# Performance work log

Hardware: AMD Instinct MI355X
Metric: run time of the kernel (lower is better)

The kernel has to match this reference:

```python
import jax, jax.numpy as jnp
import numpy as np

B, N, D = 4, 1024, 1024
H, HD, G = 16, 64, 4          # num_heads, dim_heads, num_groups
KVH = H // G                   # kv heads = 4


def setup_inputs() -> dict:
    key = jax.random.key(0)
    ks = jax.random.split(key, 5)
    s = 0.02
    return {
        "x": jax.random.normal(ks[0], (B, N, D), jnp.float32),
        "Wq": jax.random.normal(ks[1], (D, H * HD), jnp.float32) * s,
        "Wkv": jax.random.normal(ks[2], (D, 2 * H * HD // G), jnp.float32) * s,
        "Wg": jax.random.normal(ks[3], (D, H * HD), jnp.float32) * s,
        "bg": jnp.zeros((H * HD,), jnp.float32),
        "Wo": jax.random.normal(ks[4], (H * HD, D), jnp.float32) * s,
    }


def reference(x, Wq, Wkv, Wg, bg, Wo):
    # QKV projections (no bias on q/kv/o; bias on gate)
    q = (x @ Wq).reshape(B, N, H, HD).transpose(0, 2, 1, 3)        # (B,H,N,HD)
    kv = x @ Wkv                                                    # (B,N,2*KVH*HD)
    k, v = jnp.split(kv, 2, axis=-1)
    k = k.reshape(B, N, KVH, HD).transpose(0, 2, 1, 3)             # (B,KVH,N,HD)
    v = v.reshape(B, N, KVH, HD).transpose(0, 2, 1, 3)
    # GQA: repeat_interleave kv heads to match query heads
    k = jnp.repeat(k, G, axis=1)                                    # (B,H,N,HD)
    v = jnp.repeat(v, G, axis=1)
    # scaled dot product attention
    scores = jnp.einsum("bhqd,bhkd->bhqk", q, k) / jnp.sqrt(jnp.float32(HD))
    attn = jax.nn.softmax(scores, axis=-1)
    out = jnp.einsum("bhqk,bhkd->bhqd", attn, v)                    # (B,H,N,HD)
    out = out.transpose(0, 2, 1, 3).reshape(B, N, H * HD)
    # elementwise gate then output projection
    gate = x @ Wg + bg
    return (gate * out) @ Wo
```

## Files before the change

### kernel.cpp

```cpp
#include <hip/hip_runtime.h>
#include <hip/hip_bf16.h>
#include <stdint.h>

#define BB 4
#define NN 1024
#define DD 1024
#define HH 16
#define HDIM 64
#define KVHH 4
#define MM (BB * NN)

typedef __hip_bfloat16 bf16;
typedef __attribute__((ext_vector_type(8))) short bf16x8;
typedef __attribute__((ext_vector_type(4))) float f32x4;

__device__ __forceinline__ float b2f(unsigned short u) {
  return __uint_as_float(((unsigned)u) << 16);
}
__device__ __forceinline__ unsigned short f2b(float x) {
  bf16 h = __float2bfloat16(x);
  unsigned short u;
  __builtin_memcpy(&u, &h, 2);
  return u;
}
__device__ __forceinline__ f32x4 mfma16(bf16x8 a, bf16x8 b, f32x4 c) {
  return __builtin_amdgcn_mfma_f32_16x16x32_bf16(a, b, c, 0, 0, 0);
}
__device__ __forceinline__ void gl_lds16(const short* g, short* l) {
  __builtin_amdgcn_global_load_lds(
      (const __attribute__((address_space(1))) unsigned*)g,
      (__attribute__((address_space(3))) unsigned*)l, 16, 0, 0);
}

__global__ __launch_bounds__(256) void cvt_f32_bf16(const float* __restrict__ src,
                                                    short* __restrict__ dst, int n4) {
  int i = blockIdx.x * 256 + threadIdx.x;
  if (i < n4) {
    float4 v = *(const float4*)&src[(size_t)i * 4];
    ushort4 o;
    o.x = f2b(v.x); o.y = f2b(v.y); o.z = f2b(v.z); o.w = f2b(v.w);
    *(ushort4*)&dst[(size_t)i * 4] = o;
  }
}

__global__ __launch_bounds__(256) void build_bias(const float* __restrict__ bg,
                                                  float* __restrict__ bias) {
  int i = blockIdx.x * 256 + threadIdx.x;
  if (i < 2560) bias[i] = (i >= 1024 && i < 2048) ? bg[i - 1024] : 0.f;
}

__global__ __launch_bounds__(256) void transpose_w(const float* __restrict__ W,
                                                   short* __restrict__ WT, int K, int N) {
  __shared__ short T[64 * 68];
  const int tid = threadIdx.x;
  const int n0 = blockIdx.x * 64, k0 = blockIdx.y * 64;
  {
    int i0 = tid >> 4, j4 = (tid & 15) * 4;
#pragma unroll
    for (int ii = 0; ii < 4; ++ii) {
      int i = i0 + 16 * ii;
      float4 w = *(const float4*)&W[(size_t)(k0 + i) * N + n0 + j4];
      ushort4 o;
      o.x = f2b(w.x); o.y = f2b(w.y); o.z = f2b(w.z); o.w = f2b(w.w);
      *(ushort4*)&T[i * 68 + j4] = o;
    }
  }
  __syncthreads();
  {
    int n = tid >> 2, k16 = (tid & 3) * 16;
    short tmp[16];
#pragma unroll
    for (int kk = 0; kk < 16; ++kk) tmp[kk] = T[(k16 + kk) * 68 + n];
    short* dst = WT + (size_t)(n0 + n) * K + k0 + k16;
#pragma unroll
    for (int s = 0; s < 16; s += 4) *(ushort4*)&dst[s] = *(const ushort4*)&tmp[s];
  }
}

__global__ __launch_bounds__(256) void transpose_v(const short* __restrict__ qgkv,
                                                   short* __restrict__ vt) {
  __shared__ short T[64 * 68];
  const int tid = threadIdx.x;
  const int t0 = blockIdx.x * 64;
  const int b = blockIdx.y >> 2, kvh = blockIdx.y & 3;
  {
    int i0 = tid >> 4, j4 = (tid & 15) * 4;
#pragma unroll
    for (int ii = 0; ii < 4; ++ii) {
      int i = i0 + 16 * ii;
      const short* src = qgkv + (size_t)(b * NN + t0 + i) * 2560 + 2304 + kvh * 64 + j4;
      *(ushort4*)&T[i * 68 + j4] = *(const ushort4*)src;
    }
  }
  __syncthreads();
  {
    int d = tid >> 2, t16 = (tid & 3) * 16;
    short tmp[16];
#pragma unroll
    for (int tt = 0; tt < 16; ++tt) tmp[tt] = T[(t16 + tt) * 68 + d];
    short* dst = vt + (size_t)((b * KVHH + kvh) * 64 + d) * NN + t0 + t16;
#pragma unroll
    for (int s = 0; s < 16; s += 4) *(ushort4*)&dst[s] = *(const ushort4*)&tmp[s];
  }
}

__global__ __launch_bounds__(256) void gemm_mfma(
    const short* __restrict__ A, const short* __restrict__ WT,
    const float* __restrict__ bias, void* __restrict__ Cout, int K, int Nw,
    int out_is_f32) {
  __shared__ short As[128 * 32];
  __shared__ short Bs[128 * 32];
  const int tid = threadIdx.x;
  const int wave = tid >> 6, lane = tid & 63, l15 = lane & 15, quad = lane >> 4;
  const int m0 = blockIdx.y * 128, n0 = blockIdx.x * 128;
  const int wm = (wave & 1) * 64, wn = (wave >> 1) * 64;
  const int arow = tid >> 2, ac = (tid & 3) * 8;

  f32x4 acc[4][4] = {};
  for (int k0 = 0; k0 < K; k0 += 32) {
    __syncthreads();
    gl_lds16(A + (size_t)(m0 + arow) * K + k0 + ac, As + wave * 512);
    gl_lds16(A + (size_t)(m0 + arow + 64) * K + k0 + ac, As + wave * 512 + 2048);
    gl_lds16(WT + (size_t)(n0 + arow) * K + k0 + ac, Bs + wave * 512);
    gl_lds16(WT + (size_t)(n0 + arow + 64) * K + k0 + ac, Bs + wave * 512 + 2048);
    __syncthreads();
    bf16x8 af[4], bfr[4];
#pragma unroll
    for (int i = 0; i < 4; ++i)
      af[i] = *(const bf16x8*)&As[(wm + 16 * i + l15) * 32 + quad * 8];
#pragma unroll
    for (int j = 0; j < 4; ++j)
      bfr[j] = *(const bf16x8*)&Bs[(wn + 16 * j + l15) * 32 + quad * 8];
#pragma unroll
    for (int i = 0; i < 4; ++i)
#pragma unroll
      for (int j = 0; j < 4; ++j) acc[i][j] = mfma16(af[i], bfr[j], acc[i][j]);
  }
#pragma unroll
  for (int j = 0; j < 4; ++j) {
    int col = n0 + wn + 16 * j + l15;
    float bv = bias ? bias[col] : 0.f;
#pragma unroll
    for (int i = 0; i < 4; ++i) {
#pragma unroll
      for (int r = 0; r < 4; ++r) {
        int row = m0 + wm + 16 * i + quad * 4 + r;
        float v = acc[i][j][r] + bv;
        if (out_is_f32)
          ((float*)Cout)[(size_t)row * Nw + col] = v;
        else
          ((unsigned short*)Cout)[(size_t)row * Nw + col] = f2b(v);
      }
    }
  }
}

__global__ __launch_bounds__(256) void gemm_mfma64(
    const short* __restrict__ A, const short* __restrict__ WT,
    const float* __restrict__ bias, void* __restrict__ Cout, int K, int Nw,
    int out_is_f32) {
  __shared__ short As[64 * 32];
  __shared__ short Bs[128 * 32];
  const int tid = threadIdx.x;
  const int wave = tid >> 6, lane = tid & 63, l15 = lane & 15, quad = lane >> 4;
  const int m0 = blockIdx.y * 64, n0 = blockIdx.x * 128;
  const int wm = (wave & 1) * 32, wn = (wave >> 1) * 64;
  const int arow = tid >> 2, ac = (tid & 3) * 8;

  f32x4 acc[2][4] = {};
  for (int k0 = 0; k0 < K; k0 += 32) {
    __syncthreads();
    gl_lds16(A + (size_t)(m0 + arow) * K + k0 + ac, As + wave * 512);
    gl_lds16(WT + (size_t)(n0 + arow) * K + k0 + ac, Bs + wave * 512);
    gl_lds16(WT + (size_t)(n0 + arow + 64) * K + k0 + ac, Bs + wave * 512 + 2048);
    __syncthreads();
    bf16x8 af[2], bfr[4];
#pragma unroll
    for (int i = 0; i < 2; ++i)
      af[i] = *(const bf16x8*)&As[(wm + 16 * i + l15) * 32 + quad * 8];
#pragma unroll
    for (int j = 0; j < 4; ++j)
      bfr[j] = *(const bf16x8*)&Bs[(wn + 16 * j + l15) * 32 + quad * 8];
#pragma unroll
    for (int i = 0; i < 2; ++i)
#pragma unroll
      for (int j = 0; j < 4; ++j) acc[i][j] = mfma16(af[i], bfr[j], acc[i][j]);
  }
#pragma unroll
  for (int j = 0; j < 4; ++j) {
    int col = n0 + wn + 16 * j + l15;
    float bv = bias ? bias[col] : 0.f;
#pragma unroll
    for (int i = 0; i < 2; ++i) {
#pragma unroll
      for (int r = 0; r < 4; ++r) {
        int row = m0 + wm + 16 * i + quad * 4 + r;
        float v = acc[i][j][r] + bv;
        if (out_is_f32)
          ((float*)Cout)[(size_t)row * Nw + col] = v;
        else
          ((unsigned short*)Cout)[(size_t)row * Nw + col] = f2b(v);
      }
    }
  }
}

__global__ __launch_bounds__(256, 4) void attn_mfma2(
    const short* __restrict__ qgkv, const short* __restrict__ vt,
    unsigned short* __restrict__ gated) {
  __shared__ short Ps[2][64 * 72];
  __shared__ float Lbuf[16 * 64];
  __shared__ float Lq[64];
  const int tid = threadIdx.x;
  const int w = tid >> 6, lane = tid & 63, l15 = lane & 15, quad = lane >> 4;
  const int qt = blockIdx.x, bh = blockIdx.y, b = bh >> 4, h = bh & 15, kvh = h >> 2;

  bf16x8 qf[4][2];
#pragma unroll
  for (int jq = 0; jq < 4; ++jq) {
    const short* qp =
        qgkv + (size_t)(b * NN + qt * 64 + 16 * jq + l15) * 2560 + h * 64 + quad * 8;
    qf[jq][0] = *(const bf16x8*)qp;
    qf[jq][1] = *(const bf16x8*)(qp + 32);
  }

  f32x4 oacc[4];
  float ls[4];
#pragma unroll
  for (int jq = 0; jq < 4; ++jq) {
    oacc[jq] = (f32x4){0.f, 0.f, 0.f, 0.f};
    ls[jq] = 0.f;
  }

  const short* kp = qgkv + (size_t)(b * NN + w * 16 + l15) * 2560 + 2048 + kvh * 64 + quad * 8;
  const short* vp = vt + (size_t)((b * KVHH + kvh) * 64 + 16 * w + l15) * NN + quad * 8;

  for (int kt = 0; kt < 16; ++kt) {
    bf16x8 kf0 = *(const bf16x8*)kp;
    bf16x8 kf1 = *(const bf16x8*)(kp + 32);
    kp += 64 * 2560;
    short* pb = &Ps[kt & 1][0];
#pragma unroll
    for (int jq = 0; jq < 4; ++jq) {
      f32x4 st = mfma16(kf0, qf[jq][0], (f32x4){0.f, 0.f, 0.f, 0.f});
      st = mfma16(kf1, qf[jq][1], st);
      float p0 = __expf(st[0] * 0.125f);
      float p1 = __expf(st[1] * 0.125f);
      float p2 = __expf(st[2] * 0.125f);
      float p3 = __expf(st[3] * 0.125f);
      ls[jq] += (p0 + p1) + (p2 + p3);
      uint2 dd;
      dd.x = (unsigned)f2b(p0) | ((unsigned)f2b(p1) << 16);
      dd.y = (unsigned)f2b(p2) | ((unsigned)f2b(p3) << 16);
      *(uint2*)&pb[(16 * jq + l15) * 72 + w * 16 + 4 * quad] = dd;
    }
    __syncthreads();
    bf16x8 vf0 = *(const bf16x8*)vp;
    bf16x8 vf1 = *(const bf16x8*)(vp + 32);
    vp += 64;
#pragma unroll
    for (int jq = 0; jq < 4; ++jq) {
      bf16x8 pf0 = *(const bf16x8*)&pb[(16 * jq + l15) * 72 + quad * 8];
      bf16x8 pf1 = *(const bf16x8*)&pb[(16 * jq + l15) * 72 + 32 + quad * 8];
      oacc[jq] = mfma16(pf0, vf0, oacc[jq]);
      oacc[jq] = mfma16(pf1, vf1, oacc[jq]);
    }
  }

#pragma unroll
  for (int jq = 0; jq < 4; ++jq)
    Lbuf[(w * 4 + quad) * 64 + jq * 16 + l15] = ls[jq];
  __syncthreads();
  if (tid < 64) {
    float s = 0.f;
#pragma unroll
    for (int i = 0; i < 16; ++i) s += Lbuf[i * 64 + tid];
    Lq[tid] = s;
  }
  __syncthreads();

#pragma unroll
  for (int jq = 0; jq < 4; ++jq) {
#pragma unroll
    for (int r = 0; r < 4; ++r) {
      int qloc = 16 * jq + 4 * quad + r;
      float lv = Lq[qloc];
      size_t row = (size_t)(b * NN + qt * 64 + qloc);
      float gv = b2f(((const unsigned short*)qgkv)[row * 2560 + 1024 + h * 64 + 16 * w + l15]);
      gated[row * 1024 + h * 64 + 16 * w + l15] = f2b(oacc[jq][r] / lv * gv);
    }
  }
}

extern "C" void kernel_launch(void* const* d_in, const int* in_sizes, int n_in,
                              void* d_out, int out_size, void* d_ws,
                              size_t ws_size, hipStream_t stream) {
  const float* x = (const float*)d_in[0];
  const float* Wq = (const float*)d_in[1];
  const float* Wkv = (const float*)d_in[2];
  const float* Wg = (const float*)d_in[3];
  const float* bg = (const float*)d_in[4];
  const float* Wo = (const float*)d_in[5];
  float* out = (float*)d_out;

  short* ws = (short*)d_ws;
  short* xb = ws;
  short* WcT = xb + 4194304;
  short* WoT = WcT + 2621440;
  short* qgkv = WoT + 1048576;
  short* vtw = qgkv + 10485760;
  float* bias_f32 = (float*)(vtw + 1048576);

  dim3 blk(256);
  cvt_f32_bf16<<<4096, blk, 0, stream>>>(x, xb, 1048576);
  transpose_w<<<dim3(16, 16), blk, 0, stream>>>(Wq, WcT, 1024, 1024);
  transpose_w<<<dim3(16, 16), blk, 0, stream>>>(Wg, WcT + 1024 * 1024, 1024, 1024);
  transpose_w<<<dim3(8, 16), blk, 0, stream>>>(Wkv, WcT + 2048 * 1024, 1024, 512);
  transpose_w<<<dim3(16, 16), blk, 0, stream>>>(Wo, WoT, 1024, 1024);
  build_bias<<<10, blk, 0, stream>>>(bg, bias_f32);

  gemm_mfma<<<dim3(20, 32), blk, 0, stream>>>(xb, WcT, bias_f32, qgkv, 1024, 2560, 0);
  transpose_v<<<dim3(16, 16), blk, 0, stream>>>(qgkv, vtw);
  attn_mfma2<<<dim3(16, 64), blk, 0, stream>>>(qgkv, vtw, (unsigned short*)xb);
  gemm_mfma64<<<dim3(8, 64), blk, 0, stream>>>(xb, WoT, nullptr, out, 1024, 1024, 1);
}
```

Measured before the change: 194.5 us.

## Stage K/V through swizzled LDS double-buffer, fuse V transpose and weight transposes

The attention kernel now prefetches K and V tiles into double-buffered, XOR-swizzled shared memory with async global-to-LDS loads, replacing direct per-lane global loads. The row-sum reduction uses wave shuffles instead of a large LDS buffer. The QKV GEMM epilogue writes V directly in transposed layout, removing the separate transpose_v kernel, and the four weight transposes are merged into one launch. The aims are to hide global load latency in attention and to cut launch overhead and one extra pass over V. In exchange, occupancy is lowered to 3 blocks per SM, and the V epilogue writes are strided and uncoalesced.

Measured after the change: 191.9 us. Within noise of the previous version (-1.3%).

```diff
diff --git a/kernel.cpp b/kernel.cpp
--- a/kernel.cpp
+++ b/kernel.cpp
@@ -49,8 +49,22 @@
   if (i < 2560) bias[i] = (i >= 1024 && i < 2048) ? bg[i - 1024] : 0.f;
 }
 
-__global__ __launch_bounds__(256) void transpose_w(const float* __restrict__ W,
-                                                   short* __restrict__ WT, int K, int N) {
+__global__ __launch_bounds__(256) void transpose_all(
+    const float* __restrict__ Wq, const float* __restrict__ Wkv,
+    const float* __restrict__ Wg, const float* __restrict__ Wo,
+    short* __restrict__ WcT, short* __restrict__ WoT) {
+  const int z = blockIdx.z;
+  const float* W;
+  short* WT;
+  int N = 1024;
+  const int K = 1024;
+  if (z == 0) { W = Wq; WT = WcT; }
+  else if (z == 1) { W = Wg; WT = WcT + 1048576; }
+  else if (z == 2) {
+    W = Wkv; WT = WcT + 2097152; N = 512;
+    if (blockIdx.x >= 8) return;
+  } else { W = Wo; WT = WoT; }
+
   __shared__ short T[64 * 68];
   const int tid = threadIdx.x;
   const int n0 = blockIdx.x * 64, k0 = blockIdx.y * 64;
@@ -77,37 +91,10 @@
   }
 }
 
-__global__ __launch_bounds__(256) void transpose_v(const short* __restrict__ qgkv,
-                                                   short* __restrict__ vt) {
-  __shared__ short T[64 * 68];
-  const int tid = threadIdx.x;
-  const int t0 = blockIdx.x * 64;
-  const int b = blockIdx.y >> 2, kvh = blockIdx.y & 3;
-  {
-    int i0 = tid >> 4, j4 = (tid & 15) * 4;
-#pragma unroll
-    for (int ii = 0; ii < 4; ++ii) {
-      int i = i0 + 16 * ii;
-      const short* src = qgkv + (size_t)(b * NN + t0 + i) * 2560 + 2304 + kvh * 64 + j4;
-      *(ushort4*)&T[i * 68 + j4] = *(const ushort4*)src;
-    }
-  }
-  __syncthreads();
-  {
-    int d = tid >> 2, t16 = (tid & 3) * 16;
-    short tmp[16];
-#pragma unroll
-    for (int tt = 0; tt < 16; ++tt) tmp[tt] = T[(t16 + tt) * 68 + d];
-    short* dst = vt + (size_t)((b * KVHH + kvh) * 64 + d) * NN + t0 + t16;
-#pragma unroll
-    for (int s = 0; s < 16; s += 4) *(ushort4*)&dst[s] = *(const ushort4*)&tmp[s];
-  }
-}
-
 __global__ __launch_bounds__(256) void gemm_mfma(
     const short* __restrict__ A, const short* __restrict__ WT,
     const float* __restrict__ bias, void* __restrict__ Cout, int K, int Nw,
-    int out_is_f32) {
+    int out_is_f32, short* __restrict__ vt) {
   __shared__ short As[128 * 32];
   __shared__ short Bs[128 * 32];
   const int tid = threadIdx.x;
@@ -140,16 +127,22 @@
   for (int j = 0; j < 4; ++j) {
     int col = n0 + wn + 16 * j + l15;
     float bv = bias ? bias[col] : 0.f;
+    const bool is_v = (vt != nullptr) && (col >= 2304);
+    int kvh = (col - 2304) >> 6, d = (col - 2304) & 63;
 #pragma unroll
     for (int i = 0; i < 4; ++i) {
 #pragma unroll
       for (int r = 0; r < 4; ++r) {
         int row = m0 + wm + 16 * i + quad * 4 + r;
         float v = acc[i][j][r] + bv;
-        if (out_is_f32)
+        if (is_v) {
+          int b = row >> 10, tok = row & 1023;
+          vt[((size_t)((b * 4 + kvh) * 64 + d)) * 1024 + tok] = (short)f2b(v);
+        } else if (out_is_f32) {
           ((float*)Cout)[(size_t)row * Nw + col] = v;
-        else
+        } else {
           ((unsigned short*)Cout)[(size_t)row * Nw + col] = f2b(v);
+        }
       }
     }
   }
@@ -205,15 +198,20 @@
   }
 }
 
-__global__ __launch_bounds__(256, 4) void attn_mfma2(
+__global__ __launch_bounds__(256, 3) void attn_mfma3(
     const short* __restrict__ qgkv, const short* __restrict__ vt,
     unsigned short* __restrict__ gated) {
-  __shared__ short Ps[2][64 * 72];
-  __shared__ float Lbuf[16 * 64];
+  __shared__ short Kt[2][64 * 64];
+  __shared__ short Vt[2][64 * 64];
+  __shared__ short Ps[64 * 64];
+  __shared__ float Lpart[4 * 64];
   __shared__ float Lq[64];
   const int tid = threadIdx.x;
   const int w = tid >> 6, lane = tid & 63, l15 = lane & 15, quad = lane >> 4;
   const int qt = blockIdx.x, bh = blockIdx.y, b = bh >> 4, h = bh & 15, kvh = h >> 2;
+  const int fs = l15 & 7;
+  const int s0 = (quad ^ fs) * 8;
+  const int s1 = ((4 + quad) ^ fs) * 8;
 
   bf16x8 qf[4][2];
 #pragma unroll
@@ -224,6 +222,13 @@
     qf[jq][1] = *(const bf16x8*)(qp + 32);
   }
 
+  const int srow = lane >> 3;
+  const int schunk = (lane & 7) ^ srow;
+  const short* kstage =
+      qgkv + (size_t)(b * NN + 16 * w + srow) * 2560 + 2048 + kvh * 64 + schunk * 8;
+  const short* vstage =
+      vt + (size_t)((b * KVHH + kvh) * 64 + 16 * w + srow) * 1024 + schunk * 8;
+
   f32x4 oacc[4];
   float ls[4];
 #pragma unroll
@@ -232,14 +237,20 @@
     ls[jq] = 0.f;
   }
 
-  const short* kp = qgkv + (size_t)(b * NN + w * 16 + l15) * 2560 + 2048 + kvh * 64 + quad * 8;
-  const short* vp = vt + (size_t)((b * KVHH + kvh) * 64 + 16 * w + l15) * NN + quad * 8;
+  const int pslot = ((2 * w + (quad >> 1)) ^ fs) * 8 + (quad & 1) * 4;
+
+  {
+    gl_lds16(kstage, &Kt[0][(16 * w) * 64]);
+    gl_lds16(kstage + 20480, &Kt[0][(16 * w + 8) * 64]);
+    gl_lds16(vstage, &Vt[0][(16 * w) * 64]);
+    gl_lds16(vstage + 8192, &Vt[0][(16 * w + 8) * 64]);
+  }
 
   for (int kt = 0; kt < 16; ++kt) {
-    bf16x8 kf0 = *(const bf16x8*)kp;
-    bf16x8 kf1 = *(const bf16x8*)(kp + 32);
-    kp += 64 * 2560;
-    short* pb = &Ps[kt & 1][0];
+    const int cur = kt & 1;
+    __syncthreads();
+    bf16x8 kf0 = *(const bf16x8*)&Kt[cur][(16 * w + l15) * 64 + s0];
+    bf16x8 kf1 = *(const bf16x8*)&Kt[cur][(16 * w + l15) * 64 + s1];
 #pragma unroll
     for (int jq = 0; jq < 4; ++jq) {
       f32x4 st = mfma16(kf0, qf[jq][0], (f32x4){0.f, 0.f, 0.f, 0.f});
@@ -252,31 +263,40 @@
       uint2 dd;
       dd.x = (unsigned)f2b(p0) | ((unsigned)f2b(p1) << 16);
       dd.y = (unsigned)f2b(p2) | ((unsigned)f2b(p3) << 16);
-      *(uint2*)&pb[(16 * jq + l15) * 72 + w * 16 + 4 * quad] = dd;
-    }
-    __syncthreads();
-    bf16x8 vf0 = *(const bf16x8*)vp;
-    bf16x8 vf1 = *(const bf16x8*)(vp + 32);
-    vp += 64;
+      *(uint2*)&Ps[(16 * jq + l15) * 64 + pslot] = dd;
+    }
+    __syncthreads();
+    if (kt < 15) {
+      const short* kp = kstage + (size_t)(kt + 1) * 163840;
+      const short* vp = vstage + (size_t)(kt + 1) * 64;
+      gl_lds16(kp, &Kt[1 - cur][(16 * w) * 64]);
+      gl_lds16(kp + 20480, &Kt[1 - cur][(16 * w + 8) * 64]);
+      gl_lds16(vp, &Vt[1 - cur][(16 * w) * 64]);
+      gl_lds16(vp + 8192, &Vt[1 - cur][(16 * w + 8) * 64]);
+    }
+    bf16x8 vf0 = *(const bf16x8*)&Vt[cur][(16 * w + l15) * 64 + s0];
+    bf16x8 vf1 = *(const bf16x8*)&Vt[cur][(16 * w + l15) * 64 + s1];
 #pragma unroll
     for (int jq = 0; jq < 4; ++jq) {
-      bf16x8 pf0 = *(const bf16x8*)&pb[(16 * jq + l15) * 72 + quad * 8];
-      bf16x8 pf1 = *(const bf16x8*)&pb[(16 * jq + l15) * 72 + 32 + quad * 8];
+      bf16x8 pf0 = *(const bf16x8*)&Ps[(16 * jq + l15) * 64 + s0];
+      bf16x8 pf1 = *(const bf16x8*)&Ps[(16 * jq + l15) * 64 + s1];
       oacc[jq] = mfma16(pf0, vf0, oacc[jq]);
       oacc[jq] = mfma16(pf1, vf1, oacc[jq]);
     }
   }
 
 #pragma unroll
-  for (int jq = 0; jq < 4; ++jq)
-    Lbuf[(w * 4 + quad) * 64 + jq * 16 + l15] = ls[jq];
+  for (int jq = 0; jq < 4; ++jq) {
+    ls[jq] += __shfl_xor(ls[jq], 16);
+    ls[jq] += __shfl_xor(ls[jq], 32);
+  }
+  if (quad == 0) {
+#pragma unroll
+    for (int jq = 0; jq < 4; ++jq) Lpart[w * 64 + 16 * jq + l15] = ls[jq];
+  }
   __syncthreads();
-  if (tid < 64) {
-    float s = 0.f;
-#pragma unroll
-    for (int i = 0; i < 16; ++i) s += Lbuf[i * 64 + tid];
-    Lq[tid] = s;
-  }
+  if (tid < 64)
+    Lq[tid] = Lpart[tid] + Lpart[64 + tid] + Lpart[128 + tid] + Lpart[192 + tid];
   __syncthreads();
 
 #pragma unroll
@@ -313,14 +333,10 @@
 
   dim3 blk(256);
   cvt_f32_bf16<<<4096, blk, 0, stream>>>(x, xb, 1048576);
-  transpose_w<<<dim3(16, 16), blk, 0, stream>>>(Wq, WcT, 1024, 1024);
-  transpose_w<<<dim3(16, 16), blk, 0, stream>>>(Wg, WcT + 1024 * 1024, 1024, 1024);
-  transpose_w<<<dim3(8, 16), blk, 0, stream>>>(Wkv, WcT + 2048 * 1024, 1024, 512);
-  transpose_w<<<dim3(16, 16), blk, 0, stream>>>(Wo, WoT, 1024, 1024);
+  transpose_all<<<dim3(16, 16, 4), blk, 0, stream>>>(Wq, Wkv, Wg, Wo, WcT, WoT);
   build_bias<<<10, blk, 0, stream>>>(bg, bias_f32);
 
-  gemm_mfma<<<dim3(20, 32), blk, 0, stream>>>(xb, WcT, bias_f32, qgkv, 1024, 2560, 0);
-  transpose_v<<<dim3(16, 16), blk, 0, stream>>>(qgkv, vtw);
-  attn_mfma2<<<dim3(16, 64), blk, 0, stream>>>(qgkv, vtw, (unsigned short*)xb);
+  gemm_mfma<<<dim3(20, 32), blk, 0, stream>>>(xb, WcT, bias_f32, qgkv, 1024, 2560, 0, vtw);
+  attn_mfma3<<<dim3(16, 64), blk, 0, stream>>>(qgkv, vtw, (unsigned short*)xb);
   gemm_mfma64<<<dim3(8, 64), blk, 0, stream>>>(xb, WoT, nullptr, out, 1024, 1024, 1);
 }
```
